# Optimization experiments

Hardware: AMD Instinct MI355X
Metric: run time of the kernel (lower is better)

## Reference

```python
import jax, jax.numpy as jnp
import numpy as np


def _conv1x1(x, w, b):
    # x: (B, C, H, W), w: (O, C), b: (O,)  -> (B, O, H, W)
    return jnp.einsum('oc,bchw->bohw', w, x) + b[None, :, None, None]


def _branch(xq, xkv, wq, bq, wk, bk, wv, bv):
    B, C, H, W = xq.shape
    N = H * W
    q = _conv1x1(xq, wq, bq).reshape(B, -1, N)   # (B, d, N)
    k = _conv1x1(xkv, wk, bk).reshape(B, -1, N)  # (B, d, N)
    v = _conv1x1(xkv, wv, bv).reshape(B, C, N)   # (B, C, N)
    energy = jnp.einsum('bdi,bdj->bij', q, k)    # (B, N, N), no scale (as in source)
    attn = jax.nn.softmax(energy, axis=-1)
    out = jnp.einsum('bcj,bij->bci', v, attn)    # bmm(v, attn^T)
    return out.reshape(B, C, H, W)


def setup_inputs() -> dict:
    key = jax.random.key(0)
    ks = jax.random.split(key, 16)
    B, C, H, W = 4, 256, 64, 64
    d = C // 8
    s_in = 0.02
    inp = {
        'x1': jax.random.normal(ks[0], (B, C, H, W), jnp.float32),
        'x2': jax.random.normal(ks[1], (B, C, H, W), jnp.float32),
        'wq1': jax.random.normal(ks[2], (d, C), jnp.float32) * s_in,
        'bq1': jnp.zeros((d,), jnp.float32),
        'wk1': jax.random.normal(ks[3], (d, C), jnp.float32) * s_in,
        'bk1': jnp.zeros((d,), jnp.float32),
        'wv1': jax.random.normal(ks[4], (C, C), jnp.float32) * s_in,
        'bv1': jnp.zeros((C,), jnp.float32),
        'wq2': jax.random.normal(ks[5], (d, C), jnp.float32) * s_in,
        'bq2': jnp.zeros((d,), jnp.float32),
        'wk2': jax.random.normal(ks[6], (d, C), jnp.float32) * s_in,
        'bk2': jnp.zeros((d,), jnp.float32),
        'wv2': jax.random.normal(ks[7], (C, C), jnp.float32) * s_in,
        'bv2': jnp.zeros((C,), jnp.float32),
    }
    return inp


def reference(x1, x2, wq1, bq1, wk1, bk1, wv1, bv1, wq2, bq2, wk2, bk2, wv2, bv2):
    out1 = _branch(x1, x2, wq1, bq1, wk1, bk1, wv1, bv1)
    out2 = _branch(x1, x2, wq2, bq2, wk2, bk2, wv2, bv2)
    return x1 + x2 + out1 + out2
```

## Files before the change

### kernel.cpp

```cpp
#include <hip/hip_runtime.h>
#include <hip/hip_fp8.h>

#define N_TOK 4096
#define C_DIM 256
#define D_DIM 32

typedef float f32x4 __attribute__((ext_vector_type(4)));
typedef short short8 __attribute__((ext_vector_type(8)));
typedef unsigned short u16;
typedef unsigned char u8;
typedef long long i64;

__device__ __forceinline__ u16 f2bf(float f) {
    unsigned int u = __builtin_bit_cast(unsigned int, f);
    u += 0x7fffu + ((u >> 16) & 1u);
    return (u16)(u >> 16);
}
__device__ __forceinline__ float bf2f(u16 h) {
    unsigned int u = ((unsigned int)h) << 16;
    return __builtin_bit_cast(float, u);
}
__device__ __forceinline__ float exp2_fast(float x) {
#if __has_builtin(__builtin_amdgcn_exp2f)
    return __builtin_amdgcn_exp2f(x);
#else
    return exp2f(x);
#endif
}
template<bool HI>
__device__ __forceinline__ int pk_fp8(float a, float b, int old) {
#if __has_builtin(__builtin_amdgcn_cvt_pk_fp8_f32)
    return __builtin_amdgcn_cvt_pk_fp8_f32(a, b, old, HI);
#else
    __hip_fp8_e4m3 fa(a), fb(b);
    int v = (int)fa.__x | ((int)fb.__x << 8);
    return HI ? ((old & 0xffff) | (v << 16)) : ((old & ~0xffff) | (v & 0xffff));
#endif
}
__device__ __forceinline__ u8 f2fp8(float f) {
    return (u8)(pk_fp8<false>(f, f, 0) & 0xff);
}


__global__ __launch_bounds__(256) void qk_proj(
    const float* __restrict__ x1, const float* __restrict__ x2,
    const float* __restrict__ wq1, const float* __restrict__ bq1,
    const float* __restrict__ wk1, const float* __restrict__ bk1,
    const float* __restrict__ wq2, const float* __restrict__ bq2,
    const float* __restrict__ wk2, const float* __restrict__ bk2,
    u16* __restrict__ wsQ, u16* __restrict__ wsK)
{
    __shared__ float w_lds[32 * 256];
    const int ib = blockIdx.x;
    const int comb = blockIdx.y;
    const int b = comb & 3;
    const int branch = (comb >> 2) & 1;
    const int qk = comb >> 3;

    const float* x = qk ? x2 : x1;
    const float* w; const float* bias; u16* dst;
    if (qk == 0) { w = branch ? wq2 : wq1; bias = branch ? bq2 : bq1; dst = wsQ; }
    else         { w = branch ? wk2 : wk1; bias = branch ? bk2 : bk1; dst = wsK; }
    const int slice = branch * 4 + b;
    dst += (size_t)slice * N_TOK * D_DIM;
    const float osc = (qk == 0) ? 1.44269504088896341f : 1.0f;

    const int tid = threadIdx.x;
    for (int t = tid; t < 32 * 256; t += 256) w_lds[t] = w[t];
    __syncthreads();

    const int il = tid & 63;
    const int db = tid >> 6;
    const float* xc = x + (size_t)b * C_DIM * N_TOK + ib * 64 + il;

    float acc[8] = {0.f,0.f,0.f,0.f,0.f,0.f,0.f,0.f};
    for (int c4 = 0; c4 < 256; c4 += 4) {
        const float xv0 = xc[(size_t)(c4 + 0) * N_TOK];
        const float xv1 = xc[(size_t)(c4 + 1) * N_TOK];
        const float xv2 = xc[(size_t)(c4 + 2) * N_TOK];
        const float xv3 = xc[(size_t)(c4 + 3) * N_TOK];
#pragma unroll
        for (int mm = 0; mm < 8; ++mm) {
            const float4 wv = *(const float4*)&w_lds[(db * 8 + mm) * 256 + c4];
            acc[mm] += xv0 * wv.x + xv1 * wv.y + xv2 * wv.z + xv3 * wv.w;
        }
    }
    short8 pack;
#pragma unroll
    for (int mm = 0; mm < 8; ++mm)
        pack[mm] = (short)f2bf((acc[mm] + bias[db * 8 + mm]) * osc);
    *(short8*)(dst + (size_t)(ib * 64 + il) * D_DIM + db * 8) = pack;
}

__device__ __forceinline__ void stage_xt(u16* xtb, const float* xb, int ks,
                                         int wave, int lane)
{
    const int j  = (wave & 1) * 64 + lane;
    const int cb = (wave >> 1) * 16;
    const float* xp = xb + (size_t)(ks * 32 + cb) * N_TOK + j;
    u16 vals[16];
#pragma unroll
    for (int qq = 0; qq < 16; ++qq) vals[qq] = f2bf(xp[(size_t)qq * N_TOK]);
    const int swz = (j >> 1) & 3;
    u16* row = xtb + j * 32;
    const int c0 = cb >> 3;
    *(short8*)&row[((c0    ) ^ swz) * 8] = *(const short8*)&vals[0];
    *(short8*)&row[((c0 + 1) ^ swz) * 8] = *(const short8*)&vals[8];
}

__global__ __launch_bounds__(256, 2) void v_proj(
    const float* __restrict__ x2,
    const float* __restrict__ wv1, const float* __restrict__ bv1,
    const float* __restrict__ wv2, const float* __restrict__ bv2,
    u8* __restrict__ wsV)
{
    __shared__ __align__(16) u16 wl[128 * 256];
    __shared__ __align__(16) u16 xt[2][128 * 32];

    const int jt = blockIdx.x, ct = blockIdx.y, s = blockIdx.z;
    const int branch = s >> 2, b = s & 3;
    const float* w    = branch ? wv2 : wv1;
    const float* bias = branch ? bv2 : bv1;
    u8* dstB = wsV + (size_t)s * N_TOK * C_DIM;
    const float* xb = x2 + (size_t)b * C_DIM * N_TOK + jt * 128;

    const int tid = threadIdx.x;
    const int wave = tid >> 6, lane = tid & 63;
    const int wr = wave >> 1, wc = wave & 1;
    const int g = lane >> 4, li = lane & 15;

    {
        const int c = tid >> 1;
        const int kh = (tid & 1) * 128;
        const float* wrow = w + (size_t)(ct * 128 + c) * C_DIM + kh;
        u16* lrow = wl + c * 256;
#pragma unroll
        for (int kk = 0; kk < 128; kk += 8) {
            const float4 a0 = *(const float4*)&wrow[kk];
            const float4 a1 = *(const float4*)&wrow[kk + 4];
            u16 tmp[8] = {f2bf(a0.x), f2bf(a0.y), f2bf(a0.z), f2bf(a0.w),
                          f2bf(a1.x), f2bf(a1.y), f2bf(a1.z), f2bf(a1.w)};
            const int kc = (kh + kk) >> 3;
            *(short8*)&lrow[(kc ^ (c & 7)) * 8] = *(const short8*)tmp;
        }
    }
    stage_xt(&xt[0][0], xb, 0, wave, lane);
    __syncthreads();

    f32x4 acc[4][4];
#pragma unroll
    for (int mf = 0; mf < 4; ++mf)
#pragma unroll
        for (int nf = 0; nf < 4; ++nf) acc[mf][nf] = (f32x4){0.f, 0.f, 0.f, 0.f};

    int buf = 0;
    for (int ks = 0; ks < 8; ++ks) {
        if (ks < 7) stage_xt(&xt[buf ^ 1][0], xb, ks + 1, wave, lane);

        short8 af[4], bf[4];
#pragma unroll
        for (int mf = 0; mf < 4; ++mf) {
            const int c = wr * 64 + mf * 16 + li;
            af[mf] = *(const short8*)&wl[c * 256 + (((ks * 4 + g) ^ (li & 7)) * 8)];
        }
#pragma unroll
        for (int nf = 0; nf < 4; ++nf) {
            const int j = wc * 64 + nf * 16 + li;
            bf[nf] = *(const short8*)&xt[buf][j * 32 + ((g ^ ((j >> 1) & 3)) * 8)];
        }
        __builtin_amdgcn_s_setprio(1);
#pragma unroll
        for (int mf = 0; mf < 4; ++mf)
#pragma unroll
            for (int nf = 0; nf < 4; ++nf)
                acc[mf][nf] = __builtin_amdgcn_mfma_f32_16x16x32_bf16(
                    af[mf], bf[nf], acc[mf][nf], 0, 0, 0);
        __builtin_amdgcn_s_setprio(0);
        __syncthreads();
        buf ^= 1;
    }

#pragma unroll
    for (int mf = 0; mf < 4; ++mf) {
#pragma unroll
        for (int r = 0; r < 4; ++r) {
            const int c = ct * 128 + wr * 64 + mf * 16 + 4 * g + r;
            const float bv = bias[c];
#pragma unroll
            for (int nf = 0; nf < 4; ++nf) {
                const int j = jt * 128 + wc * 64 + nf * 16 + li;
                dstB[(size_t)(j >> 5) * 8192 + ((j >> 3) & 3) * 2048
                     + c * 8 + (j & 7)] = f2fp8(acc[mf][nf][r] + bv);
            }
        }
    }
}

__global__ __launch_bounds__(256, 4) void attn_fwd(
    const u16* __restrict__ Q, const u16* __restrict__ K,
    const u8* __restrict__ V, u16* __restrict__ O)
{
    __shared__ __align__(16) u8 vlds[2][2][4096];
    __shared__ float lscr[2][2][64][2];

    const int n  = blockIdx.x;
    const int s  = n & 7;
    const int ib = (n >> 3) & 63;
    const int ct = n >> 9;
    const u16* q = Q + (size_t)s * N_TOK * D_DIM;
    const u16* k = K + (size_t)s * N_TOK * D_DIM;
    const u8*  v = V + (size_t)s * N_TOK * C_DIM + ct * 1024;
    u16*       o = O + (size_t)s * N_TOK * C_DIM + ct * 128;

    const int tid  = threadIdx.x;
    const int wave = tid >> 6;
    const int lane = tid & 63;
    const int grp  = wave >> 1;
    const int wg   = wave & 1;
    const int g    = lane >> 4;
    const int li   = lane & 15;
    const int i0   = ib * 64 + wg * 32;
    const int jbase = grp * (N_TOK / 2);
    const int NP = N_TOK / 2 / 32;

    short8 qf[2];
    qf[0] = *(const short8*)(q + (size_t)(i0 + li) * D_DIM + 8 * g);
    qf[1] = *(const short8*)(q + (size_t)(i0 + 16 + li) * D_DIM + 8 * g);

    f32x4 acc[2][8];
#pragma unroll
    for (int it = 0; it < 2; ++it)
#pragma unroll
        for (int cf = 0; cf < 8; ++cf) acc[it][cf] = (f32x4){0.f, 0.f, 0.f, 0.f};
    float lsum[2] = {0.f, 0.f};

    {
        const u8* tile = v + (size_t)(jbase >> 5) * 8192;
#pragma unroll
        for (int ii = 0; ii < 2; ++ii) {
            const int pc = wg * 2 + ii;
            __builtin_amdgcn_global_load_lds(
                (const __attribute__((address_space(1))) void*)(tile + pc * 2048 + lane * 16),
                (__attribute__((address_space(3))) void*)(&vlds[grp][0][0] + pc * 1024),
                16, 0, 0);
        }
    }
    short8 keC = *(const short8*)(k + (size_t)(jbase + 2 * li    ) * D_DIM + 8 * g);
    short8 koC = *(const short8*)(k + (size_t)(jbase + 2 * li + 1) * D_DIM + 8 * g);
    __syncthreads();

    const f32x4 z = (f32x4){0.f, 0.f, 0.f, 0.f};
    i64 paC[2];
#pragma unroll
    for (int it = 0; it < 2; ++it) {
        f32x4 se = __builtin_amdgcn_mfma_f32_16x16x32_bf16(keC, qf[it], z, 0, 0, 0);
        f32x4 so = __builtin_amdgcn_mfma_f32_16x16x32_bf16(koC, qf[it], z, 0, 0, 0);
        float pe[4], po[4];
#pragma unroll
        for (int r = 0; r < 4; ++r) { pe[r] = exp2_fast(se[r]); po[r] = exp2_fast(so[r]); }
        lsum[it] += ((pe[0] + po[0]) + (pe[1] + po[1])) + ((pe[2] + po[2]) + (pe[3] + po[3]));
        int w0 = pk_fp8<false>(pe[0], po[0], 0);
        w0     = pk_fp8<true >(pe[1], po[1], w0);
        int w1 = pk_fp8<false>(pe[2], po[2], 0);
        w1     = pk_fp8<true >(pe[3], po[3], w1);
        paC[it] = (i64)(((unsigned long long)(unsigned)w1 << 32) | (unsigned)w0);
    }
    keC = *(const short8*)(k + (size_t)(jbase + 32 + 2 * li    ) * D_DIM + 8 * g);
    koC = *(const short8*)(k + (size_t)(jbase + 32 + 2 * li + 1) * D_DIM + 8 * g);

    int buf = 0;
    for (int p = 0; p < NP; ++p) {
        const bool more = (p + 1 < NP);
        short8 keN, koN;
        f32x4 se0, so0, se1, so1;
        if (more) {
            const u8* tile = v + (size_t)((jbase + (p + 1) * 32) >> 5) * 8192;
            u8* dst = &vlds[grp][buf ^ 1][0];
#pragma unroll
            for (int ii = 0; ii < 2; ++ii) {
                const int pc = wg * 2 + ii;
                __builtin_amdgcn_global_load_lds(
                    (const __attribute__((address_space(1))) void*)(tile + pc * 2048 + lane * 16),
                    (__attribute__((address_space(3))) void*)(dst + pc * 1024),
                    16, 0, 0);
            }
            if (p + 2 < NP) {
                const int j2 = jbase + (p + 2) * 32;
                keN = *(const short8*)(k + (size_t)(j2 + 2 * li    ) * D_DIM + 8 * g);
                koN = *(const short8*)(k + (size_t)(j2 + 2 * li + 1) * D_DIM + 8 * g);
            }
            se0 = __builtin_amdgcn_mfma_f32_16x16x32_bf16(keC, qf[0], z, 0, 0, 0);
            so0 = __builtin_amdgcn_mfma_f32_16x16x32_bf16(koC, qf[0], z, 0, 0, 0);
            se1 = __builtin_amdgcn_mfma_f32_16x16x32_bf16(keC, qf[1], z, 0, 0, 0);
            so1 = __builtin_amdgcn_mfma_f32_16x16x32_bf16(koC, qf[1], z, 0, 0, 0);
        }

        {
            const u8* vb = &vlds[grp][buf][0];
            const i64* vbL = (const i64*)(vb + g * 1024 + li * 8);
            __builtin_amdgcn_s_setprio(1);
#pragma unroll
            for (int cf = 0; cf < 8; ++cf) {
                const i64 vfL = vbL[cf * 16];
                acc[0][cf] = __builtin_amdgcn_mfma_f32_16x16x32_fp8_fp8(paC[0], vfL, acc[0][cf], 0, 0, 0);
                acc[1][cf] = __builtin_amdgcn_mfma_f32_16x16x32_fp8_fp8(paC[1], vfL, acc[1][cf], 0, 0, 0);
            }
            __builtin_amdgcn_s_setprio(0);
        }

        if (more) {
#pragma unroll
            for (int it = 0; it < 2; ++it) {
                const f32x4 se = it ? se1 : se0;
                const f32x4 so = it ? so1 : so0;
                float pe[4], po[4];
#pragma unroll
                for (int r = 0; r < 4; ++r) { pe[r] = exp2_fast(se[r]); po[r] = exp2_fast(so[r]); }
                lsum[it] += ((pe[0] + po[0]) + (pe[1] + po[1]))
                          + ((pe[2] + po[2]) + (pe[3] + po[3]));
                int w0 = pk_fp8<false>(pe[0], po[0], 0);
                w0     = pk_fp8<true >(pe[1], po[1], w0);
                int w1 = pk_fp8<false>(pe[2], po[2], 0);
                w1     = pk_fp8<true >(pe[3], po[3], w1);
                paC[it] = (i64)(((unsigned long long)(unsigned)w1 << 32) | (unsigned)w0);
            }
            keC = keN; koC = koN;
        }
        __syncthreads();
        buf ^= 1;
    }

#pragma unroll
    for (int it = 0; it < 2; ++it) {
        lsum[it] += __shfl_xor(lsum[it], 16);
        lsum[it] += __shfl_xor(lsum[it], 32);
        lscr[grp][wg][lane][it] = lsum[it];
    }

    f32x4* pv = (f32x4*)&vlds[0][0][0];
#pragma unroll
    for (int it = 0; it < 2; ++it) {
        __syncthreads();
        if (grp == 1) {
#pragma unroll
            for (int cf = 0; cf < 8; ++cf)
                pv[(wg * 8 + cf) * 64 + lane] = acc[it][cf];
        }
        __syncthreads();
        if (grp == 0) {
#pragma unroll
            for (int cf = 0; cf < 8; ++cf) {
                const f32x4 o4 = pv[(wg * 8 + cf) * 64 + lane];
                acc[it][cf][0] += o4[0]; acc[it][cf][1] += o4[1];
                acc[it][cf][2] += o4[2]; acc[it][cf][3] += o4[3];
            }
        }
    }

    if (grp == 0) {
#pragma unroll
        for (int it = 0; it < 2; ++it) {
            const float linv = 1.0f / (lscr[0][wg][lane][it] + lscr[1][wg][lane][it]);
            float lr[4];
#pragma unroll
            for (int r = 0; r < 4; ++r) lr[r] = __shfl(linv, 4 * g + r);
#pragma unroll
            for (int cf = 0; cf < 8; ++cf)
#pragma unroll
                for (int r = 0; r < 4; ++r)
                    o[(size_t)(i0 + it * 16 + 4 * g + r) * C_DIM + cf * 16 + li] =
                        f2bf(acc[it][cf][r] * lr[r]);
        }
    }
}

__global__ __launch_bounds__(256) void epilogue(
    const float* __restrict__ x1, const float* __restrict__ x2,
    const u16* __restrict__ O, float* __restrict__ out)
{
    __shared__ float tl[64][65];
    const int it = blockIdx.x, ct = blockIdx.y, b = blockIdx.z;
    const int tid = threadIdx.x;
    const int cl = tid & 63, r0 = tid >> 6;

    const u16* O1 = O + (size_t)(b)     * N_TOK * C_DIM;
    const u16* O2 = O + (size_t)(4 + b) * N_TOK * C_DIM;

#pragma unroll
    for (int rr = 0; rr < 16; ++rr) {
        const int il = r0 + rr * 4;
        const size_t off = (size_t)(it * 64 + il) * C_DIM + ct * 64 + cl;
        tl[il][cl] = bf2f(O1[off]) + bf2f(O2[off]);
    }
    __syncthreads();
#pragma unroll
    for (int rr = 0; rr < 16; ++rr) {
        const int c2 = r0 + rr * 4;
        const size_t idx = ((size_t)b * C_DIM + ct * 64 + c2) * N_TOK + it * 64 + cl;
        out[idx] = x1[idx] + x2[idx] + tl[cl][c2];
    }
}

extern "C" void kernel_launch(void* const* d_in, const int* in_sizes, int n_in,
                              void* d_out, int out_size, void* d_ws, size_t ws_size,
                              hipStream_t stream)
{
    const float* x1  = (const float*)d_in[0];
    const float* x2  = (const float*)d_in[1];
    const float* wq1 = (const float*)d_in[2];
    const float* bq1 = (const float*)d_in[3];
    const float* wk1 = (const float*)d_in[4];
    const float* bk1 = (const float*)d_in[5];
    const float* wv1 = (const float*)d_in[6];
    const float* bv1 = (const float*)d_in[7];
    const float* wq2 = (const float*)d_in[8];
    const float* bq2 = (const float*)d_in[9];
    const float* wk2 = (const float*)d_in[10];
    const float* bk2 = (const float*)d_in[11];
    const float* wv2 = (const float*)d_in[12];
    const float* bv2 = (const float*)d_in[13];
    float* out = (float*)d_out;

    u16* wsQ = (u16*)d_ws;
    u16* wsK = wsQ + (size_t)8 * N_TOK * D_DIM;
    u8*  wsV = (u8*)(wsK + (size_t)8 * N_TOK * D_DIM);
    u16* wsO = (u16*)(wsV + (size_t)8 * N_TOK * C_DIM);

    qk_proj<<<dim3(64, 16), 256, 0, stream>>>(x1, x2, wq1, bq1, wk1, bk1,
                                              wq2, bq2, wk2, bk2, wsQ, wsK);
    v_proj<<<dim3(32, 2, 8), 256, 0, stream>>>(x2, wv1, bv1, wv2, bv2, wsV);
    attn_fwd<<<dim3(1024), 256, 0, stream>>>(wsQ, wsK, wsV, wsO);
    epilogue<<<dim3(64, 4, 4), 256, 0, stream>>>(x1, x2, wsO, out);
}
```

Measured before the change: 145.5 us.

## Share softmax probabilities across both channel halves via LDS in attention kernel

The attention block grows to 512 threads and covers all 256 value channels instead of launching separate blocks per 128-channel half. Only the first channel-wave set computes QK^T, exp and the fp8 packing, then hands the packed probabilities to the second set through a double-buffered LDS array. This removes the duplicated QK and exp work across channel tiles. In exchange it adds LDS traffic and a serial dependency on the producer waves, halves the grid to 512 blocks, and drops the K prefetch that ran two steps ahead.

```diff
diff --git a/kernel.cpp b/kernel.cpp
--- a/kernel.cpp
+++ b/kernel.cpp
@@ -196,26 +196,27 @@
     }
 }
 
-__global__ __launch_bounds__(256, 4) void attn_fwd(
+__global__ __launch_bounds__(512, 4) void attn_fwd(
     const u16* __restrict__ Q, const u16* __restrict__ K,
     const u8* __restrict__ V, u16* __restrict__ O)
 {
-    __shared__ __align__(16) u8 vlds[2][2][4096];
+    __shared__ __align__(16) u8  vlds[2][2][2][4096];
+    __shared__ __align__(16) i64 palds[2][2][2][64][2];
     __shared__ float lscr[2][2][64][2];
 
     const int n  = blockIdx.x;
     const int s  = n & 7;
-    const int ib = (n >> 3) & 63;
-    const int ct = n >> 9;
+    const int ib = n >> 3;
     const u16* q = Q + (size_t)s * N_TOK * D_DIM;
     const u16* k = K + (size_t)s * N_TOK * D_DIM;
-    const u8*  v = V + (size_t)s * N_TOK * C_DIM + ct * 1024;
-    u16*       o = O + (size_t)s * N_TOK * C_DIM + ct * 128;
+    const u8*  v = V + (size_t)s * N_TOK * C_DIM;
+    u16*       o = O + (size_t)s * N_TOK * C_DIM;
 
     const int tid  = threadIdx.x;
     const int wave = tid >> 6;
     const int lane = tid & 63;
-    const int grp  = wave >> 1;
+    const int cw   = wave >> 2;
+    const int grp  = (wave >> 1) & 1;
     const int wg   = wave & 1;
     const int g    = lane >> 4;
     const int li   = lane & 15;
@@ -223,80 +224,89 @@
     const int jbase = grp * (N_TOK / 2);
     const int NP = N_TOK / 2 / 32;
 
-    short8 qf[2];
-    qf[0] = *(const short8*)(q + (size_t)(i0 + li) * D_DIM + 8 * g);
-    qf[1] = *(const short8*)(q + (size_t)(i0 + 16 + li) * D_DIM + 8 * g);
-
     f32x4 acc[2][8];
 #pragma unroll
     for (int it = 0; it < 2; ++it)
 #pragma unroll
         for (int cf = 0; cf < 8; ++cf) acc[it][cf] = (f32x4){0.f, 0.f, 0.f, 0.f};
     float lsum[2] = {0.f, 0.f};
+    const f32x4 z = (f32x4){0.f, 0.f, 0.f, 0.f};
+
+    short8 qf[2];
+    short8 keC, koC;
+    i64 paC[2];
 
     {
-        const u8* tile = v + (size_t)(jbase >> 5) * 8192;
+        const int c2a = wave * 2;
 #pragma unroll
         for (int ii = 0; ii < 2; ++ii) {
-            const int pc = wg * 2 + ii;
+            const int c2 = c2a + ii;
+            const int gC = c2 >> 3, cwc = (c2 >> 2) & 1, pch = c2 & 3;
+            const u8* src = v + (size_t)(gC * 64) * 8192 + pch * 2048 + cwc * 1024
+                              + lane * 16;
             __builtin_amdgcn_global_load_lds(
-                (const __attribute__((address_space(1))) void*)(tile + pc * 2048 + lane * 16),
-                (__attribute__((address_space(3))) void*)(&vlds[grp][0][0] + pc * 1024),
+                (const __attribute__((address_space(1))) void*)src,
+                (__attribute__((address_space(3))) void*)(&vlds[gC][cwc][0][pch * 1024]),
                 16, 0, 0);
         }
     }
-    short8 keC = *(const short8*)(k + (size_t)(jbase + 2 * li    ) * D_DIM + 8 * g);
-    short8 koC = *(const short8*)(k + (size_t)(jbase + 2 * li + 1) * D_DIM + 8 * g);
+    if (cw == 0) {
+        qf[0] = *(const short8*)(q + (size_t)(i0 + li) * D_DIM + 8 * g);
+        qf[1] = *(const short8*)(q + (size_t)(i0 + 16 + li) * D_DIM + 8 * g);
+        keC = *(const short8*)(k + (size_t)(jbase + 2 * li    ) * D_DIM + 8 * g);
+        koC = *(const short8*)(k + (size_t)(jbase + 2 * li + 1) * D_DIM + 8 * g);
+    }
     __syncthreads();
-
-    const f32x4 z = (f32x4){0.f, 0.f, 0.f, 0.f};
-    i64 paC[2];
-#pragma unroll
-    for (int it = 0; it < 2; ++it) {
-        f32x4 se = __builtin_amdgcn_mfma_f32_16x16x32_bf16(keC, qf[it], z, 0, 0, 0);
-        f32x4 so = __builtin_amdgcn_mfma_f32_16x16x32_bf16(koC, qf[it], z, 0, 0, 0);
-        float pe[4], po[4];
-#pragma unroll
-        for (int r = 0; r < 4; ++r) { pe[r] = exp2_fast(se[r]); po[r] = exp2_fast(so[r]); }
-        lsum[it] += ((pe[0] + po[0]) + (pe[1] + po[1])) + ((pe[2] + po[2]) + (pe[3] + po[3]));
-        int w0 = pk_fp8<false>(pe[0], po[0], 0);
-        w0     = pk_fp8<true >(pe[1], po[1], w0);
-        int w1 = pk_fp8<false>(pe[2], po[2], 0);
-        w1     = pk_fp8<true >(pe[3], po[3], w1);
-        paC[it] = (i64)(((unsigned long long)(unsigned)w1 << 32) | (unsigned)w0);
-    }
-    keC = *(const short8*)(k + (size_t)(jbase + 32 + 2 * li    ) * D_DIM + 8 * g);
-    koC = *(const short8*)(k + (size_t)(jbase + 32 + 2 * li + 1) * D_DIM + 8 * g);
+    if (cw == 0) {
+#pragma unroll
+        for (int it = 0; it < 2; ++it) {
+            f32x4 se = __builtin_amdgcn_mfma_f32_16x16x32_bf16(keC, qf[it], z, 0, 0, 0);
+            f32x4 so = __builtin_amdgcn_mfma_f32_16x16x32_bf16(koC, qf[it], z, 0, 0, 0);
+            float pe[4], po[4];
+#pragma unroll
+            for (int r = 0; r < 4; ++r) { pe[r] = exp2_fast(se[r]); po[r] = exp2_fast(so[r]); }
+            lsum[it] += ((pe[0] + po[0]) + (pe[1] + po[1]))
+                      + ((pe[2] + po[2]) + (pe[3] + po[3]));
+            int w0 = pk_fp8<false>(pe[0], po[0], 0);
+            w0     = pk_fp8<true >(pe[1], po[1], w0);
+            int w1 = pk_fp8<false>(pe[2], po[2], 0);
+            w1     = pk_fp8<true >(pe[3], po[3], w1);
+            paC[it] = (i64)(((unsigned long long)(unsigned)w1 << 32) | (unsigned)w0);
+        }
+        palds[grp][wg][0][lane][0] = paC[0];
+        palds[grp][wg][0][lane][1] = paC[1];
+    }
+    __syncthreads();
 
     int buf = 0;
     for (int p = 0; p < NP; ++p) {
         const bool more = (p + 1 < NP);
-        short8 keN, koN;
-        f32x4 se0, so0, se1, so1;
         if (more) {
-            const u8* tile = v + (size_t)((jbase + (p + 1) * 32) >> 5) * 8192;
-            u8* dst = &vlds[grp][buf ^ 1][0];
+            const int c2a = wave * 2;
 #pragma unroll
             for (int ii = 0; ii < 2; ++ii) {
-                const int pc = wg * 2 + ii;
+                const int c2 = c2a + ii;
+                const int gC = c2 >> 3, cwc = (c2 >> 2) & 1, pch = c2 & 3;
+                const u8* src = v + (size_t)(gC * 64 + p + 1) * 8192 + pch * 2048
+                                  + cwc * 1024 + lane * 16;
                 __builtin_amdgcn_global_load_lds(
-                    (const __attribute__((address_space(1))) void*)(tile + pc * 2048 + lane * 16),
-                    (__attribute__((address_space(3))) void*)(dst + pc * 1024),
+                    (const __attribute__((address_space(1))) void*)src,
+                    (__attribute__((address_space(3))) void*)(&vlds[gC][cwc][buf ^ 1][pch * 1024]),
                     16, 0, 0);
             }
-            if (p + 2 < NP) {
-                const int j2 = jbase + (p + 2) * 32;
-                keN = *(const short8*)(k + (size_t)(j2 + 2 * li    ) * D_DIM + 8 * g);
-                koN = *(const short8*)(k + (size_t)(j2 + 2 * li + 1) * D_DIM + 8 * g);
-            }
-            se0 = __builtin_amdgcn_mfma_f32_16x16x32_bf16(keC, qf[0], z, 0, 0, 0);
-            so0 = __builtin_amdgcn_mfma_f32_16x16x32_bf16(koC, qf[0], z, 0, 0, 0);
-            se1 = __builtin_amdgcn_mfma_f32_16x16x32_bf16(keC, qf[1], z, 0, 0, 0);
-            so1 = __builtin_amdgcn_mfma_f32_16x16x32_bf16(koC, qf[1], z, 0, 0, 0);
+        }
+        if (cw == 0 && more) {
+            const int jn = jbase + (p + 1) * 32;
+            keC = *(const short8*)(k + (size_t)(jn + 2 * li    ) * D_DIM + 8 * g);
+            koC = *(const short8*)(k + (size_t)(jn + 2 * li + 1) * D_DIM + 8 * g);
+        }
+        if (cw == 1) {
+            paC[0] = palds[grp][wg][buf][lane][0];
+            paC[1] = palds[grp][wg][buf][lane][1];
         }
 
         {
-            const u8* vb = &vlds[grp][buf][0];
+            const u8* vb = &vlds[grp][cw][buf][0];
             const i64* vbL = (const i64*)(vb + g * 1024 + li * 8);
             __builtin_amdgcn_s_setprio(1);
 #pragma unroll
@@ -308,11 +318,11 @@
             __builtin_amdgcn_s_setprio(0);
         }
 
-        if (more) {
+        if (cw == 0 && more) {
 #pragma unroll
             for (int it = 0; it < 2; ++it) {
-                const f32x4 se = it ? se1 : se0;
-                const f32x4 so = it ? so1 : so0;
+                f32x4 se = __builtin_amdgcn_mfma_f32_16x16x32_bf16(keC, qf[it], z, 0, 0, 0);
+                f32x4 so = __builtin_amdgcn_mfma_f32_16x16x32_bf16(koC, qf[it], z, 0, 0, 0);
                 float pe[4], po[4];
 #pragma unroll
                 for (int r = 0; r < 4; ++r) { pe[r] = exp2_fast(se[r]); po[r] = exp2_fast(so[r]); }
@@ -324,33 +334,36 @@
                 w1     = pk_fp8<true >(pe[3], po[3], w1);
                 paC[it] = (i64)(((unsigned long long)(unsigned)w1 << 32) | (unsigned)w0);
             }
-            keC = keN; koC = koN;
+            palds[grp][wg][buf ^ 1][lane][0] = paC[0];
+            palds[grp][wg][buf ^ 1][lane][1] = paC[1];
         }
         __syncthreads();
         buf ^= 1;
     }
 
-#pragma unroll
-    for (int it = 0; it < 2; ++it) {
-        lsum[it] += __shfl_xor(lsum[it], 16);
-        lsum[it] += __shfl_xor(lsum[it], 32);
-        lscr[grp][wg][lane][it] = lsum[it];
-    }
-
-    f32x4* pv = (f32x4*)&vlds[0][0][0];
+    if (cw == 0) {
+#pragma unroll
+        for (int it = 0; it < 2; ++it) {
+            lsum[it] += __shfl_xor(lsum[it], 16);
+            lsum[it] += __shfl_xor(lsum[it], 32);
+            lscr[grp][wg][lane][it] = lsum[it];
+        }
+    }
+
+    f32x4* pv = (f32x4*)&vlds[0][0][0][0];
 #pragma unroll
     for (int it = 0; it < 2; ++it) {
         __syncthreads();
         if (grp == 1) {
 #pragma unroll
             for (int cf = 0; cf < 8; ++cf)
-                pv[(wg * 8 + cf) * 64 + lane] = acc[it][cf];
+                pv[(((wg << 1) | cw) * 8 + cf) * 64 + lane] = acc[it][cf];
         }
         __syncthreads();
         if (grp == 0) {
 #pragma unroll
             for (int cf = 0; cf < 8; ++cf) {
-                const f32x4 o4 = pv[(wg * 8 + cf) * 64 + lane];
+                const f32x4 o4 = pv[(((wg << 1) | cw) * 8 + cf) * 64 + lane];
                 acc[it][cf][0] += o4[0]; acc[it][cf][1] += o4[1];
                 acc[it][cf][2] += o4[2]; acc[it][cf][3] += o4[3];
             }
@@ -368,7 +381,7 @@
             for (int cf = 0; cf < 8; ++cf)
 #pragma unroll
                 for (int r = 0; r < 4; ++r)
-                    o[(size_t)(i0 + it * 16 + 4 * g + r) * C_DIM + cf * 16 + li] =
+                    o[(size_t)(i0 + it * 16 + 4 * g + r) * C_DIM + cw * 128 + cf * 16 + li] =
                         f2bf(acc[it][cf][r] * lr[r]);
         }
     }
@@ -429,6 +442,6 @@
     qk_proj<<<dim3(64, 16), 256, 0, stream>>>(x1, x2, wq1, bq1, wk1, bk1,
                                               wq2, bq2, wk2, bk2, wsQ, wsK);
     v_proj<<<dim3(32, 2, 8), 256, 0, stream>>>(x2, wv1, bv1, wv2, bv2, wsV);
-    attn_fwd<<<dim3(1024), 256, 0, stream>>>(wsQ, wsK, wsV, wsO);
+    attn_fwd<<<dim3(512), 512, 0, stream>>>(wsQ, wsK, wsV, wsO);
     epilogue<<<dim3(64, 4, 4), 256, 0, stream>>>(x1, x2, wsO, out);
 }
```

Result: slower. 151.2 us (+3.9%).
